# Optimization experiments

Hardware: AMD Instinct MI355X
Metric: run time of the kernel (lower is better)

Reference implementation:

```python
import jax, jax.numpy as jnp
import numpy as np

H_OUT = 512
W_OUT = 512


def _leaky(x):
    return jnp.where(x >= 0, x, 0.2 * x)


def _spline(cp, out_size):
    # cp: [B, R, N] control points -> [B, R, out_size] cubic Hermite interp
    N = cp.shape[-1]
    nseg = N - 1
    eps = 1e-3
    t = jnp.linspace(eps, 1.0 - eps, out_size)
    ts = t * nseg
    seg = jnp.clip(jnp.floor(ts).astype(jnp.int32), 0, nseg - 1)
    tau = jnp.clip(ts - seg.astype(ts.dtype), 0.0, 0.9999)
    t2 = tau * tau
    t3 = t2 * tau
    h00 = 2 * t3 - 3 * t2 + 1
    h10 = t3 - 2 * t2 + tau
    h01 = -2 * t3 + 3 * t2
    h11 = t3 - t2
    # central-difference tangents, scaled by 1/num_segments
    m = jnp.concatenate([
        (cp[..., 1:2] - cp[..., 0:1]) * 0.5,
        (cp[..., 2:] - cp[..., :-2]) * 0.5,
        (cp[..., -1:] - cp[..., -2:-1]) * 0.5,
    ], axis=-1) / nseg
    seg1 = jnp.clip(seg + 1, 0, N - 1)
    pk = cp[..., seg]
    pk1 = cp[..., seg1]
    mk = m[..., seg]
    mk1 = m[..., seg1]
    return h00 * pk + h10 * mk + h01 * pk1 + h11 * mk1


def _gen(feats, w1, b1, w2, b2):
    # batched per-rank 2-layer MLP: feats [B,R,D], w1 [R,D,Hd], w2 [R,Hd,C]
    hdn = _leaky(jnp.einsum('brd,rdh->brh', feats, w1) + b1[None])
    return jnp.einsum('brh,rhc->brc', hdn, w2) + b2[None]


def setup_inputs() -> dict:
    key = jax.random.key(0)
    ks = iter(jax.random.split(key, 40))
    def rn(shape, s=0.05):
        return jax.random.normal(next(ks), shape, jnp.float32) * s
    B, D, Hd = 64, 768, 256
    Rm, Ra, CX, CY = 16, 8, 24, 24
    Rt = Rm + Ra
    inp = {
        'h': jax.random.normal(next(ks), (B, D), jnp.float32),
        'rank_emb': rn((Rt, Hd), 0.1),
        'st_w1': rn((D, 2 * Hd)), 'st_b1': jnp.zeros((2 * Hd,), jnp.float32),
        'st_w2': rn((2 * Hd, Hd)), 'st_b2': jnp.zeros((Hd,), jnp.float32),
        'rm_w1': rn((Rt, 2 * Hd, Hd)), 'rm_b1': jnp.zeros((Rt, Hd), jnp.float32),
        'rm_w2': rn((Rt, Hd, Hd)), 'rm_b2': jnp.zeros((Rt, Hd), jnp.float32),
        'mx_w1': rn((Rm, Hd, Hd)), 'mx_b1': jnp.zeros((Rm, Hd), jnp.float32),
        'mx_w2': rn((Rm, Hd, CX)), 'mx_b2': jnp.zeros((Rm, CX), jnp.float32),
        'my_w1': rn((Rm, Hd, Hd)), 'my_b1': jnp.zeros((Rm, Hd), jnp.float32),
        'my_w2': rn((Rm, Hd, CY)), 'my_b2': jnp.zeros((Rm, CY), jnp.float32),
        'ax_w1': rn((Ra, Hd, Hd)), 'ax_b1': jnp.zeros((Ra, Hd), jnp.float32),
        'ax_w2': rn((Ra, Hd, CX)), 'ax_b2': jnp.zeros((Ra, CX), jnp.float32),
        'ay_w1': rn((Ra, Hd, Hd)), 'ay_b1': jnp.zeros((Ra, Hd), jnp.float32),
        'ay_w2': rn((Ra, Hd, CY)), 'ay_b2': jnp.zeros((Ra, CY), jnp.float32),
        'mult_w': jnp.ones((Rm,), jnp.float32) / Rm,
        'addx_w': jnp.ones((Ra,), jnp.float32) / Ra * 0.5,
        'addy_w': jnp.ones((Ra,), jnp.float32) / Ra * 0.5,
        'gbias': jnp.asarray(0.5, jnp.float32),
    }
    return inp


def reference(h, rank_emb, st_w1, st_b1, st_w2, st_b2,
              rm_w1, rm_b1, rm_w2, rm_b2,
              mx_w1, mx_b1, mx_w2, mx_b2,
              my_w1, my_b1, my_w2, my_b2,
              ax_w1, ax_b1, ax_w2, ax_b2,
              ay_w1, ay_b1, ay_w2, ay_b2,
              mult_w, addx_w, addy_w, gbias):
    B = h.shape[0]
    Rt = rank_emb.shape[0]
    Rm = mx_w1.shape[0]
    # shared conditioning
    shared = _leaky(h @ st_w1 + st_b1) @ st_w2 + st_b2  # [B, Hd]
    comb = jnp.concatenate([
        jnp.broadcast_to(shared[:, None, :], (B, Rt, shared.shape[-1])),
        jnp.broadcast_to(rank_emb[None], (B, Rt, rank_emb.shape[-1])),
    ], axis=-1)  # [B, Rt, 2*Hd]
    rf = _gen(comb, rm_w1, rm_b1, rm_w2, rm_b2)  # [B, Rt, Hd]
    fm, fa = rf[:, :Rm], rf[:, Rm:]
    Px_m = _gen(fm, mx_w1, mx_b1, mx_w2, mx_b2)  # [B, Rm, CX]
    Py_m = _gen(fm, my_w1, my_b1, my_w2, my_b2)
    Px_a = _gen(fa, ax_w1, ax_b1, ax_w2, ax_b2)
    Py_a = _gen(fa, ay_w1, ay_b1, ay_w2, ay_b2)
    u = _spline(Px_m, W_OUT)   # [B, Rm, W]
    v = _spline(Py_m, H_OUT)   # [B, Rm, H]
    a_x = _spline(Px_a, W_OUT)
    b_y = _spline(Py_a, H_OUT)
    depth_mult = jnp.einsum('brw,brh,r->bhw', u, v, jax.nn.softmax(mult_w))
    dx = jnp.einsum('brw,r->bw', a_x, jax.nn.softmax(addx_w))
    dy = jnp.einsum('brh,r->bh', b_y, jax.nn.softmax(addy_w))
    depth = depth_mult + dx[:, None, :] + dy[:, :, None] + gbias
    return depth[:, None]  # [B, 1, H, W]
```

## Files before the change

### kernel.cpp

```cpp
#include <hip/hip_runtime.h>


__device__ __forceinline__ float leaky(float v) { return v >= 0.f ? v : 0.2f * v; }

__global__ __launch_bounds__(256, 2) void l1_kernel(
    const float* __restrict__ h, const float* __restrict__ W,
    const float* __restrict__ bias, float* __restrict__ outp)
{
    __shared__ __align__(16) float a_lds[128][34];
    __shared__ __align__(16) float w_lds[128][34];
    const int tid = threadIdx.x;
    const int x = blockIdx.x, z = blockIdx.z;
    const int b0 = (x & 1) * 32, n0 = (x >> 1) * 32;
    const int nq = tid & 15, bq = tid >> 4;
    const int k0 = z * 128;
    float a00, a01, a10, a11;
    if (z == 0) {
        float bv0 = bias[n0 + nq * 2], bv1 = bias[n0 + nq * 2 + 1];
        a00 = bv0; a01 = bv1; a10 = bv0; a11 = bv1;
    } else { a00 = a01 = a10 = a11 = 0.f; }
    #pragma unroll
    for (int j = 0; j < 16; ++j) {
        int idx = tid + j * 256;
        int k = idx & 127, c = idx >> 7;
        a_lds[k][c] = h[(size_t)(b0 + c) * 768 + k0 + k];
        int n = idx & 31, kk = idx >> 5;
        w_lds[kk][n] = W[(size_t)(k0 + kk) * 512 + n0 + n];
    }
    __syncthreads();
    #pragma unroll 32
    for (int kk = 0; kk < 128; ++kk) {
        float2 a = *(const float2*)&a_lds[kk][bq * 2];
        float2 w = *(const float2*)&w_lds[kk][nq * 2];
        a00 += a.x * w.x; a01 += a.x * w.y;
        a10 += a.y * w.x; a11 += a.y * w.y;
    }
    float* ob = outp + (size_t)z * 32768;
    ob[(size_t)(b0 + bq * 2) * 512 + n0 + nq * 2]         = a00;
    ob[(size_t)(b0 + bq * 2) * 512 + n0 + nq * 2 + 1]     = a01;
    ob[(size_t)(b0 + bq * 2 + 1) * 512 + n0 + nq * 2]     = a10;
    ob[(size_t)(b0 + bq * 2 + 1) * 512 + n0 + nq * 2 + 1] = a11;
}

__global__ __launch_bounds__(512, 2) void l2re_kernel(
    const float* __restrict__ hid1p, const float* __restrict__ st_w2,
    const float* __restrict__ st_b2,
    const float* __restrict__ rank_emb,
    const float* __restrict__ rm_w1, const float* __restrict__ rm_b1,
    float* __restrict__ sh, float* __restrict__ re)
{
    __shared__ __align__(16) float hid_s[2][512];
    __shared__ __align__(16) float ps2[2][2][256];
    __shared__ __align__(16) float remb_s[256];
    const int tid = threadIdx.x;
    if (blockIdx.x < 32) {
        const int b0 = blockIdx.x * 2;
        if (tid < 256) {
            int row = tid >> 7, j4 = tid & 127;
            const float4* hp = (const float4*)hid1p;
            size_t off = (size_t)(b0 + row) * 128 + j4;
            float4 v0 = hp[off],         v1 = hp[8192 + off],  v2 = hp[16384 + off];
            float4 v3 = hp[24576 + off], v4 = hp[32768 + off], v5 = hp[40960 + off];
            float4 s;
            s.x = leaky(v0.x + v1.x + v2.x + v3.x + v4.x + v5.x);
            s.y = leaky(v0.y + v1.y + v2.y + v3.y + v4.y + v5.y);
            s.z = leaky(v0.z + v1.z + v2.z + v3.z + v4.z + v5.z);
            s.w = leaky(v0.w + v1.w + v2.w + v3.w + v4.w + v5.w);
            ((float4*)&hid_s[row][0])[j4] = s;
        }
        __syncthreads();
        {
            const int col = tid & 255, kg = tid >> 8;
            const int o = kg * 256;
            float a0 = 0.f, a1 = 0.f;
            const float* wp = st_w2 + (size_t)o * 256 + col;
            #pragma unroll 4
            for (int d = 0; d < 256; d += 4) {
                float w0 = wp[(size_t)(d + 0) * 256], w1 = wp[(size_t)(d + 1) * 256];
                float w2 = wp[(size_t)(d + 2) * 256], w3 = wp[(size_t)(d + 3) * 256];
                float4 s0 = *(const float4*)&hid_s[0][o + d];
                float4 s1 = *(const float4*)&hid_s[1][o + d];
                a0 += s0.x * w0 + s0.y * w1 + s0.z * w2 + s0.w * w3;
                a1 += s1.x * w0 + s1.y * w1 + s1.z * w2 + s1.w * w3;
            }
            ps2[kg][0][col] = a0; ps2[kg][1][col] = a1;
        }
        __syncthreads();
        {
            int row = tid >> 8, c = tid & 255;
            sh[(size_t)(b0 + row) * 256 + c] = st_b2[c] + ps2[0][row][c] + ps2[1][row][c];
        }
    } else {
        const int r = blockIdx.x - 32;
        if (tid < 64)
            ((float4*)remb_s)[tid] = ((const float4*)rank_emb)[(size_t)r * 64 + tid];
        __syncthreads();
        {
            const int col = tid & 255, kh = tid >> 8;
            const int o = kh * 128;
            float acc = 0.f;
            const float* wb = rm_w1 + ((size_t)r * 512 + 256 + o) * 256 + col;
            #pragma unroll 8
            for (int d = 0; d < 128; d += 4) {
                float w0 = wb[(size_t)(d + 0) * 256], w1 = wb[(size_t)(d + 1) * 256];
                float w2 = wb[(size_t)(d + 2) * 256], w3 = wb[(size_t)(d + 3) * 256];
                float4 e = *(const float4*)&remb_s[o + d];
                acc += e.x * w0 + e.y * w1 + e.z * w2 + e.w * w3;
            }
            ps2[kh][0][col] = acc;
        }
        __syncthreads();
        if (tid < 256)
            re[(size_t)r * 256 + tid] = rm_b1[r * 256 + tid] + ps2[0][0][tid] + ps2[1][0][tid];
    }
}

__global__ __launch_bounds__(512, 4) void mega_kernel(
    const float* __restrict__ sh,
    const float* __restrict__ re,
    const float* __restrict__ rm_w1,
    const float* __restrict__ rm_w2, const float* __restrict__ rm_b2,
    const float* __restrict__ mx_w1, const float* __restrict__ mx_b1,
    const float* __restrict__ mx_w2, const float* __restrict__ mx_b2,
    const float* __restrict__ my_w1, const float* __restrict__ my_b1,
    const float* __restrict__ my_w2, const float* __restrict__ my_b2,
    const float* __restrict__ ax_w1, const float* __restrict__ ax_b1,
    const float* __restrict__ ax_w2, const float* __restrict__ ax_b2,
    const float* __restrict__ ay_w1, const float* __restrict__ ay_b1,
    const float* __restrict__ ay_w2, const float* __restrict__ ay_b2,
    float* __restrict__ Pcat)
{
    __shared__ __align__(16) float sh_s[2][256];
    __shared__ __align__(16) float hdn_s[2][256];
    __shared__ __align__(16) float rf_s[2][256];
    __shared__ __align__(16) float hc_s[2][2][256];
    __shared__ __align__(16) float ps[2][2][256];
    const int tid = threadIdx.x;
    const int blk = blockIdx.x;
    const int r = blk % 24;
    const int bt = blk / 24;
    const int b0 = bt * 2;
    const int col = tid & 255, rh = tid >> 8;

    if (tid < 128)
        ((float4*)sh_s)[tid] = ((const float4*)sh)[(size_t)b0 * 64 + tid];
    __syncthreads();

    {
        float a0 = 0.f, a1 = 0.f;
        const int o = rh * 128;
        const float* wp = rm_w1 + ((size_t)r * 512 + o) * 256 + col;
        #pragma unroll 8
        for (int d = 0; d < 128; d += 4) {
            float w0 = wp[(size_t)(d + 0) * 256], w1 = wp[(size_t)(d + 1) * 256];
            float w2 = wp[(size_t)(d + 2) * 256], w3 = wp[(size_t)(d + 3) * 256];
            float4 s0 = *(const float4*)&sh_s[0][o + d];
            float4 s1 = *(const float4*)&sh_s[1][o + d];
            a0 += s0.x * w0 + s0.y * w1 + s0.z * w2 + s0.w * w3;
            a1 += s1.x * w0 + s1.y * w1 + s1.z * w2 + s1.w * w3;
        }
        ps[rh][0][col] = a0; ps[rh][1][col] = a1;
    }
    __syncthreads();
    hdn_s[rh][col] = leaky(re[(size_t)r * 256 + col] + ps[0][rh][col] + ps[1][rh][col]);
    __syncthreads();

    {
        float a0 = 0.f, a1 = 0.f;
        const int o = rh * 128;
        const float* wp = rm_w2 + (size_t)r * 65536 + (size_t)o * 256 + col;
        #pragma unroll 8
        for (int d = 0; d < 128; d += 4) {
            float w0 = wp[(size_t)(d + 0) * 256], w1 = wp[(size_t)(d + 1) * 256];
            float w2 = wp[(size_t)(d + 2) * 256], w3 = wp[(size_t)(d + 3) * 256];
            float4 s0 = *(const float4*)&hdn_s[0][o + d];
            float4 s1 = *(const float4*)&hdn_s[1][o + d];
            a0 += s0.x * w0 + s0.y * w1 + s0.z * w2 + s0.w * w3;
            a1 += s1.x * w0 + s1.y * w1 + s1.z * w2 + s1.w * w3;
        }
        ps[rh][0][col] = a0; ps[rh][1][col] = a1;
    }
    __syncthreads();
    rf_s[rh][col] = rm_b2[r * 256 + col] + ps[0][rh][col] + ps[1][rh][col];
    __syncthreads();

    const float *W1, *B1, *W2_0, *B2_0, *W2_1, *B2_1; int y0, y1;
    if (r < 16) {
        y0 = r;       y1 = 16 + r;
        W2_0 = mx_w2 + (size_t)r * 6144;  B2_0 = mx_b2 + r * 24;
        W2_1 = my_w2 + (size_t)r * 6144;  B2_1 = my_b2 + r * 24;
        W1 = (rh == 0) ? mx_w1 + (size_t)r * 65536 : my_w1 + (size_t)r * 65536;
        B1 = (rh == 0) ? mx_b1 + r * 256           : my_b1 + r * 256;
    } else {
        int rw = r - 16;
        y0 = 32 + rw;  y1 = 40 + rw;
        W2_0 = ax_w2 + (size_t)rw * 6144; B2_0 = ax_b2 + rw * 24;
        W2_1 = ay_w2 + (size_t)rw * 6144; B2_1 = ay_b2 + rw * 24;
        W1 = (rh == 0) ? ax_w1 + (size_t)rw * 65536 : ay_w1 + (size_t)rw * 65536;
        B1 = (rh == 0) ? ax_b1 + rw * 256           : ay_b1 + rw * 256;
    }

    {
        float bv = B1[col];
        float a0 = bv, a1 = bv;
        const float* wp = W1 + col;
        #pragma unroll 8
        for (int d = 0; d < 256; d += 4) {
            float w0 = wp[(size_t)(d + 0) * 256], w1 = wp[(size_t)(d + 1) * 256];
            float w2 = wp[(size_t)(d + 2) * 256], w3 = wp[(size_t)(d + 3) * 256];
            float4 s0 = *(const float4*)&rf_s[0][d];
            float4 s1 = *(const float4*)&rf_s[1][d];
            a0 += s0.x * w0 + s0.y * w1 + s0.z * w2 + s0.w * w3;
            a1 += s1.x * w0 + s1.y * w1 + s1.z * w2 + s1.w * w3;
        }
        hc_s[rh][0][col] = leaky(a0); hc_s[rh][1][col] = leaky(a1);
    }
    __syncthreads();

    float* psf = &ps[0][0][0];
    if (tid < 384) {
        int o = tid >> 2, kq = tid & 3;
        int h = o / 48, rc = o % 48;
        int row = rc / 24, cj = rc - row * 24;
        const float* wp = (h ? W2_1 : W2_0) + (size_t)(kq * 64) * 24 + cj;
        const float* hp = &hc_s[h][row][kq * 64];
        float acc = 0.f;
        #pragma unroll 8
        for (int d = 0; d < 64; d += 4) {
            float w0 = wp[(d + 0) * 24], w1 = wp[(d + 1) * 24];
            float w2 = wp[(d + 2) * 24], w3 = wp[(d + 3) * 24];
            float4 s = *(const float4*)&hp[d];
            acc += s.x * w0 + s.y * w1 + s.z * w2 + s.w * w3;
        }
        psf[tid] = acc;
    }
    __syncthreads();
    if (tid < 96) {
        int h = tid / 48, rc = tid - h * 48;
        int row = rc / 24, cj = rc - row * 24;
        float v = (h ? B2_1 : B2_0)[cj]
                + psf[tid * 4] + psf[tid * 4 + 1] + psf[tid * 4 + 2] + psf[tid * 4 + 3];
        int y = h ? y1 : y0;
        Pcat[(size_t)(b0 + row) * 1152 + y * 24 + cj] = v;
    }
}

__global__ __launch_bounds__(256, 2) void depth_fused_kernel(
    const float* __restrict__ Pcat,
    const float* __restrict__ mult_w, const float* __restrict__ addx_w,
    const float* __restrict__ addy_w, const float* __restrict__ gbias,
    float* __restrict__ out)
{
    __shared__ float cp[48][25];
    __shared__ float sw[33];
    __shared__ __align__(16) float u_s[16][132];
    __shared__ __align__(16) float v_s[16][132];
    __shared__ float dx_s[128], dy_s[128];
    const int tid = threadIdx.x;
    const int b = blockIdx.z, h0 = blockIdx.y * 128, w0 = blockIdx.x * 128;
    for (int idx = tid; idx < 1152; idx += 256)
        cp[idx / 24][idx % 24] = Pcat[(size_t)b * 1152 + idx];
    if (tid == 0) {
        float e[16], m, s;
        m = -1e30f; for (int i = 0; i < 16; ++i) m = fmaxf(m, mult_w[i]);
        s = 0.f;    for (int i = 0; i < 16; ++i) { e[i] = __expf(mult_w[i] - m); s += e[i]; }
        for (int i = 0; i < 16; ++i) sw[i] = e[i] / s;
        m = -1e30f; for (int i = 0; i < 8; ++i) m = fmaxf(m, addx_w[i]);
        s = 0.f;    for (int i = 0; i < 8; ++i) { e[i] = __expf(addx_w[i] - m); s += e[i]; }
        for (int i = 0; i < 8; ++i) sw[16 + i] = e[i] / s;
        m = -1e30f; for (int i = 0; i < 8; ++i) m = fmaxf(m, addy_w[i]);
        s = 0.f;    for (int i = 0; i < 8; ++i) { e[i] = __expf(addy_w[i] - m); s += e[i]; }
        for (int i = 0; i < 8; ++i) sw[24 + i] = e[i] / s;
        sw[32] = gbias[0];
    }
    __syncthreads();
    {
        const int local = tid & 127;
        const int gpos = (tid < 128 ? w0 : h0) + local;
        const float eps = 0.001f;
        float t = eps + (float)gpos * ((1.f - 2.f * eps) / 511.f);
        float ts = t * 23.f;
        int seg = (int)ts; if (seg > 22) seg = 22;
        float tau = ts - (float)seg;
        tau = fminf(fmaxf(tau, 0.f), 0.9999f);
        float t2 = tau * tau, t3 = t2 * tau;
        float h00 = 2.f * t3 - 3.f * t2 + 1.f;
        float h10 = t3 - 2.f * t2 + tau;
        float h01 = -2.f * t3 + 3.f * t2;
        float h11 = t3 - t2;
        int sm1 = seg > 0 ? seg - 1 : 0;
        int s1 = seg + 1;
        int sp2 = s1 < 23 ? s1 + 1 : 23;
        const float msc = 0.5f / 23.f;
        auto spl = [&](int row) -> float {
            float pk = cp[row][seg], pk1 = cp[row][s1];
            float mk  = msc * (pk1 - cp[row][sm1]);
            float mk1 = msc * (cp[row][sp2] - pk);
            return h00 * pk + h10 * mk + h01 * pk1 + h11 * mk1;
        };
        if (tid < 128) {
            #pragma unroll
            for (int r = 0; r < 16; ++r) u_s[r][local] = sw[r] * spl(r);
            float dx = sw[32];
            #pragma unroll
            for (int r = 0; r < 8; ++r) dx += sw[16 + r] * spl(32 + r);
            dx_s[local] = dx;
        } else {
            #pragma unroll
            for (int r = 0; r < 16; ++r) v_s[r][local] = spl(16 + r);
            float dy = 0.f;
            #pragma unroll
            for (int r = 0; r < 8; ++r) dy += sw[24 + r] * spl(40 + r);
            dy_s[local] = dy;
        }
    }
    __syncthreads();
    const int tw = tid & 15, th = tid >> 4;
    float acc[8][8];
    #pragma unroll
    for (int i = 0; i < 8; ++i)
        #pragma unroll
        for (int j = 0; j < 8; ++j) acc[i][j] = 0.f;
    #pragma unroll
    for (int r = 0; r < 16; ++r) {
        float4 va0 = *(const float4*)&v_s[r][th * 8];
        float4 va1 = *(const float4*)&v_s[r][th * 8 + 4];
        float4 ub0 = *(const float4*)&u_s[r][tw * 8];
        float4 ub1 = *(const float4*)&u_s[r][tw * 8 + 4];
        float va[8] = {va0.x, va0.y, va0.z, va0.w, va1.x, va1.y, va1.z, va1.w};
        float ub[8] = {ub0.x, ub0.y, ub0.z, ub0.w, ub1.x, ub1.y, ub1.z, ub1.w};
        #pragma unroll
        for (int i = 0; i < 8; ++i)
            #pragma unroll
            for (int j = 0; j < 8; ++j)
                acc[i][j] += va[i] * ub[j];
    }
    #pragma unroll
    for (int i = 0; i < 8; ++i) {
        float dyh = dy_s[th * 8 + i];
        float* op = out + (size_t)b * 262144 + (size_t)(h0 + th * 8 + i) * 512 + w0 + tw * 8;
        float4 o0, o1;
        o0.x = acc[i][0] + dx_s[tw * 8 + 0] + dyh;
        o0.y = acc[i][1] + dx_s[tw * 8 + 1] + dyh;
        o0.z = acc[i][2] + dx_s[tw * 8 + 2] + dyh;
        o0.w = acc[i][3] + dx_s[tw * 8 + 3] + dyh;
        o1.x = acc[i][4] + dx_s[tw * 8 + 4] + dyh;
        o1.y = acc[i][5] + dx_s[tw * 8 + 5] + dyh;
        o1.z = acc[i][6] + dx_s[tw * 8 + 6] + dyh;
        o1.w = acc[i][7] + dx_s[tw * 8 + 7] + dyh;
        *(float4*)op = o0;
        *(float4*)(op + 4) = o1;
    }
}

extern "C" void kernel_launch(void* const* d_in, const int* in_sizes, int n_in,
                              void* d_out, int out_size, void* d_ws, size_t ws_size,
                              hipStream_t stream) {
    const float* in_h     = (const float*)d_in[0];
    const float* rank_emb = (const float*)d_in[1];
    const float* st_w1    = (const float*)d_in[2];
    const float* st_b1    = (const float*)d_in[3];
    const float* st_w2    = (const float*)d_in[4];
    const float* st_b2    = (const float*)d_in[5];
    const float* rm_w1    = (const float*)d_in[6];
    const float* rm_b1    = (const float*)d_in[7];
    const float* rm_w2    = (const float*)d_in[8];
    const float* rm_b2    = (const float*)d_in[9];
    const float* mx_w1    = (const float*)d_in[10];
    const float* mx_b1    = (const float*)d_in[11];
    const float* mx_w2    = (const float*)d_in[12];
    const float* mx_b2    = (const float*)d_in[13];
    const float* my_w1    = (const float*)d_in[14];
    const float* my_b1    = (const float*)d_in[15];
    const float* my_w2    = (const float*)d_in[16];
    const float* my_b2    = (const float*)d_in[17];
    const float* ax_w1    = (const float*)d_in[18];
    const float* ax_b1    = (const float*)d_in[19];
    const float* ax_w2    = (const float*)d_in[20];
    const float* ax_b2    = (const float*)d_in[21];
    const float* ay_w1    = (const float*)d_in[22];
    const float* ay_b1    = (const float*)d_in[23];
    const float* ay_w2    = (const float*)d_in[24];
    const float* ay_b2    = (const float*)d_in[25];
    const float* mult_w   = (const float*)d_in[26];
    const float* addx_w   = (const float*)d_in[27];
    const float* addy_w   = (const float*)d_in[28];
    const float* gbias    = (const float*)d_in[29];
    (void)in_sizes; (void)n_in; (void)out_size; (void)ws_size;

    float* ws = (float*)d_ws;
    float* hid1p = ws;
    float* Pcat  = ws + 196608;
    float* shbuf = ws + 270336;
    float* rebuf = ws + 286720;

    l1_kernel<<<dim3(32, 1, 6), 256, 0, stream>>>(in_h, st_w1, st_b1, hid1p);

    l2re_kernel<<<56, 512, 0, stream>>>(hid1p, st_w2, st_b2,
                                        rank_emb, rm_w1, rm_b1, shbuf, rebuf);

    mega_kernel<<<768, 512, 0, stream>>>(
        shbuf, rebuf,
        rm_w1, rm_w2, rm_b2,
        mx_w1, mx_b1, mx_w2, mx_b2,
        my_w1, my_b1, my_w2, my_b2,
        ax_w1, ax_b1, ax_w2, ax_b2,
        ay_w1, ay_b1, ay_w2, ay_b2,
        Pcat);

    depth_fused_kernel<<<dim3(4, 4, 64), 256, 0, stream>>>(
        Pcat, mult_w, addx_w, addy_w, gbias, (float*)d_out);
}
```

Baseline: 246.8 us.

## Process four batch rows per mega block and split l2re across more blocks

mega_kernel now handles four batch rows per block instead of two, halving the grid to 384 blocks so each weight column loaded from global memory is reused across twice as many rows. The re vector is staged in shared memory, and the final layer-2 reduction is regrouped into two k-chunks per output. l2re_kernel is split into 176 smaller blocks, one batch row or rank per column-half, to raise parallelism in that small stage. The cost is more shared memory and registers per mega block and fewer blocks in flight, which may reduce occupancy and latency hiding.

```diff
diff --git a/kernel.cpp b/kernel.cpp
--- a/kernel.cpp
+++ b/kernel.cpp
@@ -49,16 +49,15 @@
     const float* __restrict__ rm_w1, const float* __restrict__ rm_b1,
     float* __restrict__ sh, float* __restrict__ re)
 {
-    __shared__ __align__(16) float hid_s[2][512];
-    __shared__ __align__(16) float ps2[2][2][256];
-    __shared__ __align__(16) float remb_s[256];
+    __shared__ __align__(16) float hid_s[512];
+    __shared__ __align__(16) float ps[4][128];
     const int tid = threadIdx.x;
-    if (blockIdx.x < 32) {
-        const int b0 = blockIdx.x * 2;
-        if (tid < 256) {
-            int row = tid >> 7, j4 = tid & 127;
+    const int blk = blockIdx.x;
+    if (blk < 128) {
+        const int row = blk >> 1, ch = blk & 1;
+        if (tid < 128) {
             const float4* hp = (const float4*)hid1p;
-            size_t off = (size_t)(b0 + row) * 128 + j4;
+            size_t off = (size_t)row * 128 + tid;
             float4 v0 = hp[off],         v1 = hp[8192 + off],  v2 = hp[16384 + off];
             float4 v3 = hp[24576 + off], v4 = hp[32768 + off], v5 = hp[40960 + off];
             float4 s;
@@ -66,52 +65,57 @@
             s.y = leaky(v0.y + v1.y + v2.y + v3.y + v4.y + v5.y);
             s.z = leaky(v0.z + v1.z + v2.z + v3.z + v4.z + v5.z);
             s.w = leaky(v0.w + v1.w + v2.w + v3.w + v4.w + v5.w);
-            ((float4*)&hid_s[row][0])[j4] = s;
+            ((float4*)hid_s)[tid] = s;
         }
         __syncthreads();
         {
-            const int col = tid & 255, kg = tid >> 8;
-            const int o = kg * 256;
-            float a0 = 0.f, a1 = 0.f;
+            const int c = tid & 127, kq = tid >> 7;
+            const int o = kq * 128;
+            const int col = ch * 128 + c;
+            float acc = 0.f;
             const float* wp = st_w2 + (size_t)o * 256 + col;
             #pragma unroll 4
-            for (int d = 0; d < 256; d += 4) {
+            for (int d = 0; d < 128; d += 4) {
                 float w0 = wp[(size_t)(d + 0) * 256], w1 = wp[(size_t)(d + 1) * 256];
                 float w2 = wp[(size_t)(d + 2) * 256], w3 = wp[(size_t)(d + 3) * 256];
-                float4 s0 = *(const float4*)&hid_s[0][o + d];
-                float4 s1 = *(const float4*)&hid_s[1][o + d];
-                a0 += s0.x * w0 + s0.y * w1 + s0.z * w2 + s0.w * w3;
-                a1 += s1.x * w0 + s1.y * w1 + s1.z * w2 + s1.w * w3;
+                float4 s = *(const float4*)&hid_s[o + d];
+                acc += s.x * w0 + s.y * w1 + s.z * w2 + s.w * w3;
             }
-            ps2[kg][0][col] = a0; ps2[kg][1][col] = a1;
-        }
+            ps[kq][c] = acc;
+        }
+        __syncthreads();
+        if (tid < 128) {
+            int col = ch * 128 + tid;
+            sh[(size_t)row * 256 + col] = st_b2[col]
+                + ps[0][tid] + ps[1][tid] + ps[2][tid] + ps[3][tid];
+        }
+    } else {
+        const int q = blk - 128;
+        const int r = q >> 1, ch = q & 1;
+        if (tid < 64)
+            ((float4*)hid_s)[tid] = ((const float4*)rank_emb)[(size_t)r * 64 + tid];
         __syncthreads();
         {
-            int row = tid >> 8, c = tid & 255;
-            sh[(size_t)(b0 + row) * 256 + c] = st_b2[c] + ps2[0][row][c] + ps2[1][row][c];
-        }
-    } else {
-        const int r = blockIdx.x - 32;
-        if (tid < 64)
-            ((float4*)remb_s)[tid] = ((const float4*)rank_emb)[(size_t)r * 64 + tid];
-        __syncthreads();
-        {
-            const int col = tid & 255, kh = tid >> 8;
-            const int o = kh * 128;
+            const int c = tid & 127, kq = tid >> 7;
+            const int o = kq * 64;
+            const int col = ch * 128 + c;
             float acc = 0.f;
             const float* wb = rm_w1 + ((size_t)r * 512 + 256 + o) * 256 + col;
-            #pragma unroll 8
-            for (int d = 0; d < 128; d += 4) {
+            #pragma unroll 4
+            for (int d = 0; d < 64; d += 4) {
                 float w0 = wb[(size_t)(d + 0) * 256], w1 = wb[(size_t)(d + 1) * 256];
                 float w2 = wb[(size_t)(d + 2) * 256], w3 = wb[(size_t)(d + 3) * 256];
-                float4 e = *(const float4*)&remb_s[o + d];
+                float4 e = *(const float4*)&hid_s[o + d];
                 acc += e.x * w0 + e.y * w1 + e.z * w2 + e.w * w3;
             }
-            ps2[kh][0][col] = acc;
+            ps[kq][c] = acc;
         }
         __syncthreads();
-        if (tid < 256)
-            re[(size_t)r * 256 + tid] = rm_b1[r * 256 + tid] + ps2[0][0][tid] + ps2[1][0][tid];
+        if (tid < 128) {
+            int col = ch * 128 + tid;
+            re[(size_t)r * 256 + col] = rm_b1[r * 256 + col]
+                + ps[0][tid] + ps[1][tid] + ps[2][tid] + ps[3][tid];
+        }
     }
 }
 
@@ -130,58 +134,87 @@
     const float* __restrict__ ay_w2, const float* __restrict__ ay_b2,
     float* __restrict__ Pcat)
 {
-    __shared__ __align__(16) float sh_s[2][256];
-    __shared__ __align__(16) float hdn_s[2][256];
-    __shared__ __align__(16) float rf_s[2][256];
-    __shared__ __align__(16) float hc_s[2][2][256];
-    __shared__ __align__(16) float ps[2][2][256];
+    __shared__ __align__(16) float sh_s[4][256];
+    __shared__ __align__(16) float hdn_s[4][256];
+    __shared__ __align__(16) float rf_s[4][256];
+    __shared__ __align__(16) float hc_s[2][4][256];
+    __shared__ __align__(16) float ps[2][4][256];
+    __shared__ __align__(16) float re_s[256];
     const int tid = threadIdx.x;
     const int blk = blockIdx.x;
     const int r = blk % 24;
     const int bt = blk / 24;
-    const int b0 = bt * 2;
+    const int b0 = bt * 4;
     const int col = tid & 255, rh = tid >> 8;
 
-    if (tid < 128)
+    if (tid < 256) {
         ((float4*)sh_s)[tid] = ((const float4*)sh)[(size_t)b0 * 64 + tid];
+    } else if (tid < 320) {
+        int j4 = tid - 256;
+        ((float4*)re_s)[j4] = ((const float4*)re)[(size_t)r * 64 + j4];
+    }
     __syncthreads();
 
     {
-        float a0 = 0.f, a1 = 0.f;
+        float a0 = 0.f, a1 = 0.f, a2 = 0.f, a3 = 0.f;
         const int o = rh * 128;
         const float* wp = rm_w1 + ((size_t)r * 512 + o) * 256 + col;
-        #pragma unroll 8
+        #pragma unroll 4
         for (int d = 0; d < 128; d += 4) {
             float w0 = wp[(size_t)(d + 0) * 256], w1 = wp[(size_t)(d + 1) * 256];
             float w2 = wp[(size_t)(d + 2) * 256], w3 = wp[(size_t)(d + 3) * 256];
             float4 s0 = *(const float4*)&sh_s[0][o + d];
             float4 s1 = *(const float4*)&sh_s[1][o + d];
+            float4 s2 = *(const float4*)&sh_s[2][o + d];
+            float4 s3 = *(const float4*)&sh_s[3][o + d];
             a0 += s0.x * w0 + s0.y * w1 + s0.z * w2 + s0.w * w3;
             a1 += s1.x * w0 + s1.y * w1 + s1.z * w2 + s1.w * w3;
+            a2 += s2.x * w0 + s2.y * w1 + s2.z * w2 + s2.w * w3;
+            a3 += s3.x * w0 + s3.y * w1 + s3.z * w2 + s3.w * w3;
         }
         ps[rh][0][col] = a0; ps[rh][1][col] = a1;
-    }
-    __syncthreads();
-    hdn_s[rh][col] = leaky(re[(size_t)r * 256 + col] + ps[0][rh][col] + ps[1][rh][col]);
+        ps[rh][2][col] = a2; ps[rh][3][col] = a3;
+    }
+    __syncthreads();
+    #pragma unroll
+    for (int t = 0; t < 2; ++t) {
+        int o2 = tid + t * 512;
+        int i = o2 >> 8, c = o2 & 255;
+        hdn_s[i][c] = leaky(re_s[c] + ps[0][i][c] + ps[1][i][c]);
+    }
     __syncthreads();
 
     {
-        float a0 = 0.f, a1 = 0.f;
+        float a0 = 0.f, a1 = 0.f, a2 = 0.f, a3 = 0.f;
         const int o = rh * 128;
         const float* wp = rm_w2 + (size_t)r * 65536 + (size_t)o * 256 + col;
-        #pragma unroll 8
+        #pragma unroll 4
         for (int d = 0; d < 128; d += 4) {
             float w0 = wp[(size_t)(d + 0) * 256], w1 = wp[(size_t)(d + 1) * 256];
             float w2 = wp[(size_t)(d + 2) * 256], w3 = wp[(size_t)(d + 3) * 256];
             float4 s0 = *(const float4*)&hdn_s[0][o + d];
             float4 s1 = *(const float4*)&hdn_s[1][o + d];
+            float4 s2 = *(const float4*)&hdn_s[2][o + d];
+            float4 s3 = *(const float4*)&hdn_s[3][o + d];
             a0 += s0.x * w0 + s0.y * w1 + s0.z * w2 + s0.w * w3;
             a1 += s1.x * w0 + s1.y * w1 + s1.z * w2 + s1.w * w3;
+            a2 += s2.x * w0 + s2.y * w1 + s2.z * w2 + s2.w * w3;
+            a3 += s3.x * w0 + s3.y * w1 + s3.z * w2 + s3.w * w3;
         }
         ps[rh][0][col] = a0; ps[rh][1][col] = a1;
-    }
-    __syncthreads();
-    rf_s[rh][col] = rm_b2[r * 256 + col] + ps[0][rh][col] + ps[1][rh][col];
+        ps[rh][2][col] = a2; ps[rh][3][col] = a3;
+    }
+    __syncthreads();
+    {
+        float bv;
+        #pragma unroll
+        for (int t = 0; t < 2; ++t) {
+            int o2 = tid + t * 512;
+            int i = o2 >> 8, c = o2 & 255;
+            bv = rm_b2[r * 256 + c];
+            rf_s[i][c] = bv + ps[0][i][c] + ps[1][i][c];
+        }
+    }
     __syncthreads();
 
     const float *W1, *B1, *W2_0, *B2_0, *W2_1, *B2_1; int y0, y1;
@@ -202,31 +235,36 @@
 
     {
         float bv = B1[col];
-        float a0 = bv, a1 = bv;
+        float acc0 = bv, acc1 = bv, acc2 = bv, acc3 = bv;
         const float* wp = W1 + col;
-        #pragma unroll 8
+        #pragma unroll 4
         for (int d = 0; d < 256; d += 4) {
             float w0 = wp[(size_t)(d + 0) * 256], w1 = wp[(size_t)(d + 1) * 256];
             float w2 = wp[(size_t)(d + 2) * 256], w3 = wp[(size_t)(d + 3) * 256];
             float4 s0 = *(const float4*)&rf_s[0][d];
             float4 s1 = *(const float4*)&rf_s[1][d];
-            a0 += s0.x * w0 + s0.y * w1 + s0.z * w2 + s0.w * w3;
-            a1 += s1.x * w0 + s1.y * w1 + s1.z * w2 + s1.w * w3;
-        }
-        hc_s[rh][0][col] = leaky(a0); hc_s[rh][1][col] = leaky(a1);
+            float4 s2 = *(const float4*)&rf_s[2][d];
+            float4 s3 = *(const float4*)&rf_s[3][d];
+            acc0 += s0.x * w0 + s0.y * w1 + s0.z * w2 + s0.w * w3;
+            acc1 += s1.x * w0 + s1.y * w1 + s1.z * w2 + s1.w * w3;
+            acc2 += s2.x * w0 + s2.y * w1 + s2.z * w2 + s2.w * w3;
+            acc3 += s3.x * w0 + s3.y * w1 + s3.z * w2 + s3.w * w3;
+        }
+        hc_s[rh][0][col] = leaky(acc0); hc_s[rh][1][col] = leaky(acc1);
+        hc_s[rh][2][col] = leaky(acc2); hc_s[rh][3][col] = leaky(acc3);
     }
     __syncthreads();
 
     float* psf = &ps[0][0][0];
     if (tid < 384) {
-        int o = tid >> 2, kq = tid & 3;
-        int h = o / 48, rc = o % 48;
+        int o = tid >> 1, kq = tid & 1;
+        int h = o / 96, rc = o % 96;
         int row = rc / 24, cj = rc - row * 24;
-        const float* wp = (h ? W2_1 : W2_0) + (size_t)(kq * 64) * 24 + cj;
-        const float* hp = &hc_s[h][row][kq * 64];
+        const float* wp = (h ? W2_1 : W2_0) + (size_t)(kq * 128) * 24 + cj;
+        const float* hp = &hc_s[h][row][kq * 128];
         float acc = 0.f;
-        #pragma unroll 8
-        for (int d = 0; d < 64; d += 4) {
+        #pragma unroll 4
+        for (int d = 0; d < 128; d += 4) {
             float w0 = wp[(d + 0) * 24], w1 = wp[(d + 1) * 24];
             float w2 = wp[(d + 2) * 24], w3 = wp[(d + 3) * 24];
             float4 s = *(const float4*)&hp[d];
@@ -235,11 +273,10 @@
         psf[tid] = acc;
     }
     __syncthreads();
-    if (tid < 96) {
-        int h = tid / 48, rc = tid - h * 48;
+    if (tid < 192) {
+        int h = tid / 96, rc = tid - h * 96;
         int row = rc / 24, cj = rc - row * 24;
-        float v = (h ? B2_1 : B2_0)[cj]
-                + psf[tid * 4] + psf[tid * 4 + 1] + psf[tid * 4 + 2] + psf[tid * 4 + 3];
+        float v = (h ? B2_1 : B2_0)[cj] + psf[tid * 2] + psf[tid * 2 + 1];
         int y = h ? y1 : y0;
         Pcat[(size_t)(b0 + row) * 1152 + y * 24 + cj] = v;
     }
@@ -396,10 +433,10 @@
 
     l1_kernel<<<dim3(32, 1, 6), 256, 0, stream>>>(in_h, st_w1, st_b1, hid1p);
 
-    l2re_kernel<<<56, 512, 0, stream>>>(hid1p, st_w2, st_b2,
-                                        rank_emb, rm_w1, rm_b1, shbuf, rebuf);
-
-    mega_kernel<<<768, 512, 0, stream>>>(
+    l2re_kernel<<<176, 512, 0, stream>>>(hid1p, st_w2, st_b2,
+                                         rank_emb, rm_w1, rm_b1, shbuf, rebuf);
+
+    mega_kernel<<<384, 512, 0, stream>>>(
         shbuf, rebuf,
         rm_w1, rm_w2, rm_b2,
         mx_w1, mx_b1, mx_w2, mx_b2,
```

New measurement: 228.7 us. 1.08x faster.
